# Optimization experiments

Measured on AMD Instinct MI355X. Metric: run time of the kernel, lower is better.

The kernel has to match this reference:

```python
import jax, jax.numpy as jnp
import numpy as np

B, CIN, COUT, K, H, W = 8, 256, 256, 4, 128, 128
BN_EPS = 1e-5


def setup_inputs() -> dict:
    key = jax.random.key(0)
    ks = jax.random.split(key, 12)
    n = lambda i, shape, scale: jax.random.normal(ks[i], shape, jnp.float32) * scale
    return {
        "x": jax.random.normal(ks[0], (B, CIN, H, W), jnp.float32),
        "conv_w": n(1, (COUT, CIN), 0.05),
        "conv_b": n(2, (COUT,), 0.02),
        "off_w": n(3, (K, 2, CIN), 0.02),   # k offset convs, each 1x1 -> 2 channels
        "off_b": n(4, (K, 2), 0.02),
        "wgt_w": n(5, (K, CIN), 0.05),      # weight conv 1x1 -> k channels (softmax over k)
        "wgt_b": n(6, (K,), 0.02),
        "gamma": 1.0 + n(7, (COUT,), 0.1),
        "beta": n(8, (COUT,), 0.1),
        "run_mean": n(9, (COUT,), 0.05),
        "run_var": 1.0 + 0.1 * jax.random.uniform(ks[10], (COUT,), jnp.float32),
        "out_w": n(11, (CIN, COUT), 0.05),
        "out_b": jnp.zeros((CIN,), jnp.float32),
    }


def bilinear_sample(img, gx, gy):
    """F.grid_sample(mode='bilinear', padding_mode='zeros', align_corners=True).
    img: [B,C,H,W]; gx,gy: [B,H,W] normalized coords in [-1,1]."""
    b, c, h, w = img.shape
    x = (gx + 1.0) * 0.5 * (w - 1)  # unnormalize (align_corners=True)
    y = (gy + 1.0) * 0.5 * (h - 1)
    x0 = jnp.floor(x)
    y0 = jnp.floor(y)
    wx1 = x - x0
    wy1 = y - y0
    imgf = img.reshape(b, c, h * w)

    def gather(xi, yi, wgt):
        valid = (xi >= 0) & (xi <= w - 1) & (yi >= 0) & (yi <= h - 1)
        xic = jnp.clip(xi, 0, w - 1).astype(jnp.int32)
        yic = jnp.clip(yi, 0, h - 1).astype(jnp.int32)
        idx = (yic * w + xic).reshape(b, 1, h * w)
        v = jnp.take_along_axis(imgf, idx, axis=2).reshape(b, c, h, w)
        return v * (wgt * valid)[:, None]  # zeros padding: OOB corners contribute 0

    return (gather(x0, y0, (1 - wx1) * (1 - wy1))
            + gather(x0 + 1, y0, wx1 * (1 - wy1))
            + gather(x0, y0 + 1, (1 - wx1) * wy1)
            + gather(x0 + 1, y0 + 1, wx1 * wy1))


def reference(x, conv_w, conv_b, off_w, off_b, wgt_w, wgt_b,
              gamma, beta, run_mean, run_var, out_w, out_b):
    # 1x1 projection conv
    proj = jnp.einsum('bchw,oc->bohw', x, conv_w) + conv_b[:, None, None]
    # k offset branches at once: [K,B,2,H,W]
    flows = jnp.einsum('bchw,koc->kbohw', x, off_w) + off_b[:, None, :, None, None]
    # per-branch softmax weights: [B,K,H,W]
    logits = jnp.einsum('bchw,kc->bkhw', x, wgt_w) + wgt_b[None, :, None, None]
    weights = jax.nn.softmax(logits, axis=1)
    # base grid + flow, normalized to [-1,1]
    grid_x = jnp.arange(W, dtype=jnp.float32)[None, None, None, :]  # broadcast over k,b,h
    grid_y = jnp.arange(H, dtype=jnp.float32)[None, None, :, None]
    vx = grid_x + flows[:, :, 0]  # [K,B,H,W]
    vy = grid_y + flows[:, :, 1]
    gxn = 2.0 * vx / max(W - 1, 1) - 1.0
    gyn = 2.0 * vy / max(H - 1, 1) - 1.0
    feats = jax.vmap(lambda gx, gy: bilinear_sample(proj, gx, gy))(gxn, gyn)  # [K,B,C,H,W]
    # repeat_interleave(weights, out_ch) * cat(feats) then split+sum == weighted sum over k
    fsum = jnp.einsum('kbchw,bkhw->bchw', feats, weights)
    feat = proj + fsum  # dropout in eval mode = identity
    # BatchNorm2d (eval: running stats)
    inv = gamma / jnp.sqrt(run_var + BN_EPS)
    feat = (feat - run_mean[:, None, None]) * inv[:, None, None] + beta[:, None, None]
    return jnp.einsum('bchw,oc->bohw', feat, out_w) + out_b[:, None, None]
```

## Files before the change

### kernel.cpp

```cpp
#include <hip/hip_runtime.h>
#include <cstddef>
#include <cstdint>

#define B_    8
#define CIN_  256
#define COUT_ 256
#define K_    4
#define H_    128
#define W_    128
#define HW_   (H_ * W_)
#define P_    (B_ * HW_)
#define BN_EPS 1e-5f

typedef __attribute__((ext_vector_type(8))) short bf16x8_t;
typedef __attribute__((ext_vector_type(4))) float f32x4_t;

__device__ __forceinline__ unsigned short f2bf(float f) {
    unsigned int u = __float_as_uint(f);
    u += 0x7fffu + ((u >> 16) & 1u);
    return (unsigned short)(u >> 16);
}
__device__ __forceinline__ float2 up2(unsigned int u) {
    return make_float2(__uint_as_float(u << 16), __uint_as_float(u & 0xffff0000u));
}
__device__ __forceinline__ void fma2(float2& d, float s, float2 v) {
    d.x = fmaf(s, v.x, d.x);
    d.y = fmaf(s, v.y, d.y);
}

#define GL2LDS(g, l)                                                                     \
    __builtin_amdgcn_global_load_lds((const __attribute__((address_space(1))) void*)(g), \
                                     (__attribute__((address_space(3))) void*)(l), 16, 0, 0)

__global__ __launch_bounds__(256) void k_prep(
    const float* __restrict__ conv_w, const float* __restrict__ out_w,
    const float* __restrict__ gamma, const float* __restrict__ beta,
    const float* __restrict__ rmean, const float* __restrict__ rvar,
    const float* __restrict__ out_b,
    unsigned short* __restrict__ wA, unsigned short* __restrict__ wB,
    float* __restrict__ bias2)
{
    const int t = threadIdx.x;
    if (blockIdx.x < 64) {
        const int i = (blockIdx.x * 256 + t) * 4;
        float4 a = *(const float4*)&conv_w[i];
        uint2 pa;
        pa.x = (unsigned)f2bf(a.x) | ((unsigned)f2bf(a.y) << 16);
        pa.y = (unsigned)f2bf(a.z) | ((unsigned)f2bf(a.w) << 16);
        *(uint2*)&wA[i] = pa;
    } else {
        __shared__ float sinv[256], sd[256];
        const float iv = gamma[t] * rsqrtf(rvar[t] + BN_EPS);
        sinv[t] = iv;
        sd[t]   = beta[t] - rmean[t] * iv;
        __syncthreads();
        float acc = out_b[t];
        for (int c = 0; c < 256; c += 4) {
            const float4 wv = *(const float4*)&out_w[t * 256 + c];
            acc += sd[c] * wv.x + sd[c + 1] * wv.y + sd[c + 2] * wv.z + sd[c + 3] * wv.w;
            uint2 p;
            p.x = (unsigned)f2bf(wv.x * sinv[c])     | ((unsigned)f2bf(wv.y * sinv[c + 1]) << 16);
            p.y = (unsigned)f2bf(wv.z * sinv[c + 2]) | ((unsigned)f2bf(wv.w * sinv[c + 3]) << 16);
            *(uint2*)&wB[t * 256 + c] = p;
        }
        bias2[t] = acc;
    }
}

__global__ __launch_bounds__(256) void k_flows(
    const float* __restrict__ x, const float* __restrict__ off_w,
    const float* __restrict__ off_b, const float* __restrict__ wgt_w,
    const float* __restrict__ wgt_b, unsigned short* __restrict__ xT,
    float4* __restrict__ tabW, int4* __restrict__ tabI)
{
    __shared__ float coef[12 * 256];
    __shared__ alignas(16) unsigned short tile[256 * 68];
    const int t = threadIdx.x;
    for (int idx = t; idx < 12 * 256; idx += 256)
        coef[idx] = (idx < 8 * 256) ? off_w[idx] : wgt_w[idx - 8 * 256];
    __syncthreads();

    const int p  = blockIdx.x * 256 + t;
    const int b  = p >> 14;
    const int hw = p & (HW_ - 1);
    const float* xp = x + (size_t)b * (256 * HW_) + hw;
    const int px0 = blockIdx.x * 256;

    float acc[12];
#pragma unroll
    for (int j = 0; j < 12; ++j) acc[j] = 0.f;

    for (int chunk = 0; chunk < 4; ++chunk) {
        const int cbase = chunk * 64;
#pragma unroll 4
        for (int cc = 0; cc < 64; ++cc) {
            const float xv = xp[(size_t)(cbase + cc) * HW_];
            tile[t * 68 + cc] = f2bf(xv);
#pragma unroll
            for (int j = 0; j < 12; ++j)
                acc[j] = fmaf(xv, coef[j * 256 + cbase + cc], acc[j]);
        }
        __syncthreads();
#pragma unroll
        for (int pass = 0; pass < 16; ++pass) {
            const int px = pass * 16 + (t >> 4);
            const int j4 = (t & 15) * 4;
            const uint2 v = *(const uint2*)&tile[px * 68 + j4];
            *(uint2*)&xT[(size_t)(px0 + px) * 256 + cbase + j4] = v;
        }
        __syncthreads();
    }

    const int w = hw & (W_ - 1);
    const int h = hw >> 7;
    float l[4];
#pragma unroll
    for (int k = 0; k < 4; ++k) l[k] = acc[8 + k] + wgt_b[k];
    const float m  = fmaxf(fmaxf(l[0], l[1]), fmaxf(l[2], l[3]));
    const float e0 = __expf(l[0] - m), e1 = __expf(l[1] - m);
    const float e2 = __expf(l[2] - m), e3 = __expf(l[3] - m);
    const float sinv = 1.f / (e0 + e1 + e2 + e3);
    float wk[4] = {e0 * sinv, e1 * sinv, e2 * sinv, e3 * sinv};

#pragma unroll
    for (int k = 0; k < 4; ++k) {
        const float sx = (float)w + acc[k * 2 + 0] + off_b[k * 2 + 0];
        const float sy = (float)h + acc[k * 2 + 1] + off_b[k * 2 + 1];
        const float x0f = floorf(sx), y0f = floorf(sy);
        const float fx = sx - x0f, fy = sy - y0f;
        const float vx0 = (x0f >= 0.f  && x0f <= (float)(W_ - 1)) ? 1.f : 0.f;
        const float vx1 = (x0f >= -1.f && x0f <= (float)(W_ - 2)) ? 1.f : 0.f;
        const float vy0 = (y0f >= 0.f  && y0f <= (float)(H_ - 1)) ? 1.f : 0.f;
        const float vy1 = (y0f >= -1.f && y0f <= (float)(H_ - 2)) ? 1.f : 0.f;
        const int x0 = (int)x0f, y0 = (int)y0f;
        const int cx0 = min(max(x0, 0), W_ - 1);
        const int cx1 = min(max(x0 + 1, 0), W_ - 1);
        const int cy0 = min(max(y0, 0), H_ - 1);
        const int cy1 = min(max(y0 + 1, 0), H_ - 1);
        float4 wv;
        wv.x = (1.f - fx) * (1.f - fy) * wk[k] * vx0 * vy0;
        wv.y = fx * (1.f - fy) * wk[k] * vx1 * vy0;
        wv.z = (1.f - fx) * fy * wk[k] * vx0 * vy1;
        wv.w = fx * fy * wk[k] * vx1 * vy1;
        int4 ov;
        ov.x = (cy0 * W_ + cx0) * 256;
        ov.y = (cy0 * W_ + cx1) * 256;
        ov.z = (cy1 * W_ + cx0) * 256;
        ov.w = (cy1 * W_ + cx1) * 256;
        tabW[(size_t)k * P_ + p] = wv;
        tabI[(size_t)k * P_ + p] = ov;
    }
}

#define GEMM_STAGE_AND_MFMA(A_, W_ptr_, smem_)                                              \
    char* As = smem_;                                                                       \
    char* Bs = smem_ + 16384;                                                               \
    const int w  = t >> 6;                                                                  \
    const int l  = t & 63;                                                                  \
    const int lr = l & 15;                                                                  \
    const int lq = l >> 4;                                                                  \
    f32x4_t acc[4][4];                                                                      \
    _Pragma("unroll") for (int i = 0; i < 4; ++i)                                           \
        _Pragma("unroll") for (int j = 0; j < 4; ++j)                                       \
            acc[i][j] = (f32x4_t){0.f, 0.f, 0.f, 0.f};                                      \
    const int wm = (w & 1) * 4;                                                             \
    const int wn = (w >> 1) * 4;                                                            \
    _Pragma("unroll") for (int ks = 0; ks < 4; ++ks) {                                      \
        const int k0 = ks * 64;                                                             \
        __syncthreads();                                                                    \
        _Pragma("unroll") for (int i = 0; i < 2; ++i) {                                     \
            const int mt = 2 * w + i;                                                       \
            _Pragma("unroll") for (int kc = 0; kc < 2; ++kc) {                              \
                const unsigned short* g =                                                   \
                    A_ + (size_t)(p0 + mt * 16 + lr) * 256 + k0 + kc * 32 + lq * 8;         \
                GL2LDS(g, As + (kc * 8 + mt) * 1024);                                       \
            }                                                                               \
        }                                                                                   \
        _Pragma("unroll") for (int i = 0; i < 2; ++i) {                                     \
            const int nt = 2 * w + i;                                                       \
            _Pragma("unroll") for (int kc = 0; kc < 2; ++kc) {                              \
                const unsigned short* g =                                                   \
                    W_ptr_ + (size_t)(n0 + nt * 16 + lr) * 256 + k0 + kc * 32 + lq * 8;     \
                GL2LDS(g, Bs + (kc * 8 + nt) * 1024);                                       \
            }                                                                               \
        }                                                                                   \
        __syncthreads();                                                                    \
        _Pragma("unroll") for (int kc = 0; kc < 2; ++kc) {                                  \
            bf16x8_t af[4], bfr[4];                                                         \
            _Pragma("unroll") for (int i = 0; i < 4; ++i)                                   \
                af[i] = *(const bf16x8_t*)(As + (kc * 8 + wm + i) * 1024 + l * 16);         \
            _Pragma("unroll") for (int j = 0; j < 4; ++j)                                   \
                bfr[j] = *(const bf16x8_t*)(Bs + (kc * 8 + wn + j) * 1024 + l * 16);        \
            _Pragma("unroll") for (int i = 0; i < 4; ++i)                                   \
                _Pragma("unroll") for (int j = 0; j < 4; ++j)                               \
                    acc[i][j] =                                                             \
                        __builtin_amdgcn_mfma_f32_16x16x32_bf16(af[i], bfr[j], acc[i][j],   \
                                                                0, 0, 0);                   \
        }                                                                                   \
    }

__global__ __launch_bounds__(256, 3) void k_proj(
    const unsigned short* __restrict__ A, const unsigned short* __restrict__ Wb,
    const float* __restrict__ bias, unsigned short* __restrict__ Cout)
{
    __shared__ alignas(16) char smem[33792];
    const int t  = threadIdx.x;
    const int bx = blockIdx.x;
    const int n0 = (bx & 1) * 128;
    const int p0 = (bx >> 1) * 128;

    GEMM_STAGE_AND_MFMA(A, Wb, smem)

    __syncthreads();
    unsigned short* ep = (unsigned short*)smem;
    const int mh = (w & 1) * 64, nh = (w >> 1) * 64;
#pragma unroll
    for (int j = 0; j < 4; ++j) {
        const int   col = nh + j * 16 + lr;
        const float bv  = bias[n0 + col];
#pragma unroll
        for (int i = 0; i < 4; ++i) {
#pragma unroll
            for (int r = 0; r < 4; ++r) {
                const int row = mh + i * 16 + lq * 4 + r;
                ep[row * 132 + col] = f2bf(acc[i][j][r] + bv);
            }
        }
    }
    __syncthreads();
#pragma unroll
    for (int pass = 0; pass < 16; ++pass) {
        const int row = pass * 8 + (t >> 5);
        const int c4  = (t & 31) * 4;
        const uint2 v = *(const uint2*)&ep[row * 132 + c4];
        *(uint2*)&Cout[(size_t)(p0 + row) * 256 + n0 + c4] = v;
    }
}

__global__ __launch_bounds__(256, 3) void k_out(
    const unsigned short* __restrict__ A, const unsigned short* __restrict__ Wb,
    const float* __restrict__ bias, float* __restrict__ Cout)
{
    __shared__ alignas(16) char smem[32768];
    const int t  = threadIdx.x;
    const int bx = blockIdx.x;
    const int n0 = (bx & 1) * 128;
    const int p0 = (bx >> 1) * 128;

    GEMM_STAGE_AND_MFMA(A, Wb, smem)

    const int mh = (w & 1) * 64, nh = (w >> 1) * 64;
    const int b   = p0 >> 14;
    const int hw0 = p0 & (HW_ - 1);
#pragma unroll
    for (int j = 0; j < 4; ++j) {
        const int   n  = n0 + nh + j * 16 + lr;
        const float bb = bias[n];
#pragma unroll
        for (int i = 0; i < 4; ++i) {
            f32x4_t v = acc[i][j];
            v[0] += bb; v[1] += bb; v[2] += bb; v[3] += bb;
            *(f32x4_t*)&Cout[(size_t)(b * 256 + n) * HW_ + hw0 + mh + i * 16 + lq * 4] = v;
        }
    }
}

__global__ __launch_bounds__(256) void k_sample(
    const unsigned short* __restrict__ proj, const float4* __restrict__ tabW,
    const int4* __restrict__ tabI, unsigned short* __restrict__ feat)
{
    const int t  = threadIdx.x;
    const int w  = t >> 6;
    const int l  = t & 63;
    const int ph = l >> 5;
    const int c0 = (l & 31) * 8;

    const int pbase = blockIdx.x * 16;
    const int b = pbase >> 14;
    const unsigned short* projb = proj + (size_t)b * HW_ * 256;

#pragma unroll
    for (int it = 0; it < 2; ++it) {
        const int p = pbase + it * 8 + w * 2 + ph;
        const uint4 rv = *(const uint4*)&proj[(size_t)p * 256 + c0];
        float2 a0 = up2(rv.x), a1 = up2(rv.y), a2 = up2(rv.z), a3 = up2(rv.w);
#pragma unroll
        for (int k = 0; k < 4; ++k) {
            const float4 wv = tabW[(size_t)k * P_ + p];
            const int4   ov = tabI[(size_t)k * P_ + p];
            const uint4 g0 = *(const uint4*)&projb[ov.x + c0];
            const uint4 g1 = *(const uint4*)&projb[ov.y + c0];
            const uint4 g2 = *(const uint4*)&projb[ov.z + c0];
            const uint4 g3 = *(const uint4*)&projb[ov.w + c0];
            fma2(a0, wv.x, up2(g0.x)); fma2(a1, wv.x, up2(g0.y));
            fma2(a2, wv.x, up2(g0.z)); fma2(a3, wv.x, up2(g0.w));
            fma2(a0, wv.y, up2(g1.x)); fma2(a1, wv.y, up2(g1.y));
            fma2(a2, wv.y, up2(g1.z)); fma2(a3, wv.y, up2(g1.w));
            fma2(a0, wv.z, up2(g2.x)); fma2(a1, wv.z, up2(g2.y));
            fma2(a2, wv.z, up2(g2.z)); fma2(a3, wv.z, up2(g2.w));
            fma2(a0, wv.w, up2(g3.x)); fma2(a1, wv.w, up2(g3.y));
            fma2(a2, wv.w, up2(g3.z)); fma2(a3, wv.w, up2(g3.w));
        }
        uint4 o;
        o.x = (unsigned)f2bf(a0.x) | ((unsigned)f2bf(a0.y) << 16);
        o.y = (unsigned)f2bf(a1.x) | ((unsigned)f2bf(a1.y) << 16);
        o.z = (unsigned)f2bf(a2.x) | ((unsigned)f2bf(a2.y) << 16);
        o.w = (unsigned)f2bf(a3.x) | ((unsigned)f2bf(a3.y) << 16);
        *(uint4*)&feat[(size_t)p * 256 + c0] = o;
    }
}

extern "C" void kernel_launch(void* const* d_in, const int* in_sizes, int n_in,
                              void* d_out, int out_size, void* d_ws, size_t ws_size,
                              hipStream_t stream)
{
    const float* x      = (const float*)d_in[0];
    const float* conv_w = (const float*)d_in[1];
    const float* conv_b = (const float*)d_in[2];
    const float* off_w  = (const float*)d_in[3];
    const float* off_b  = (const float*)d_in[4];
    const float* wgt_w  = (const float*)d_in[5];
    const float* wgt_b  = (const float*)d_in[6];
    const float* gamma  = (const float*)d_in[7];
    const float* beta   = (const float*)d_in[8];
    const float* rmean  = (const float*)d_in[9];
    const float* rvar   = (const float*)d_in[10];
    const float* out_w  = (const float*)d_in[11];
    const float* out_b  = (const float*)d_in[12];

    char* ws = (char*)d_ws;
    unsigned short* xT   = (unsigned short*)(ws);
    unsigned short* proj = (unsigned short*)(ws + (size_t)67108864);
    unsigned short* feat = (unsigned short*)(ws + (size_t)134217728);
    float4*         tabW = (float4*)(ws + (size_t)201326592);
    int4*           tabI = (int4*)(ws + (size_t)209715200);
    unsigned short* wA   = (unsigned short*)(ws + (size_t)218103808);
    unsigned short* wB   = (unsigned short*)(ws + (size_t)218234880);
    float*          bias2= (float*)(ws + (size_t)218365952);

    k_prep  <<<65,         256, 0, stream>>>(conv_w, out_w, gamma, beta, rmean, rvar,
                                             out_b, wA, wB, bias2);
    k_flows <<<P_ / 256,   256, 0, stream>>>(x, off_w, off_b, wgt_w, wgt_b, xT, tabW, tabI);
    k_proj  <<<(P_/128)*2, 256, 0, stream>>>(xT, wA, conv_b, proj);
    k_sample<<<P_ / 16,    256, 0, stream>>>(proj, tabW, tabI, feat);
    k_out   <<<(P_/128)*2, 256, 0, stream>>>(feat, wB, bias2, (float*)d_out);
}
```

Before: 427.9 us.

## Split channel reduction across four wave groups in k_flows and drop the LDS transpose

k_flows now handles 64 pixels per block. Each of the four wavefronts reduces a different 16-channel slice, and the partial sums for the 12 offset and weight dot products are combined through shared memory. Each thread converts its 16 channels to bf16 and writes them to xT as two 16-byte stores, which replaces the shared-memory tile transpose and its barriers. This raises parallelism and cuts LDS traffic in the stage that reads x. In exchange it adds a cross-wave reduction, lets only one wave finish the tail computation, and makes global stores less coalesced since each lane writes 32 bytes at a 512-byte stride.

```diff
diff --git a/kernel.cpp b/kernel.cpp
--- a/kernel.cpp
+++ b/kernel.cpp
@@ -73,82 +73,105 @@
     const float* __restrict__ wgt_b, unsigned short* __restrict__ xT,
     float4* __restrict__ tabW, int4* __restrict__ tabI)
 {
-    __shared__ float coef[12 * 256];
-    __shared__ alignas(16) unsigned short tile[256 * 68];
+    __shared__ float smem[3456];
     const int t = threadIdx.x;
     for (int idx = t; idx < 12 * 256; idx += 256)
-        coef[idx] = (idx < 8 * 256) ? off_w[idx] : wgt_w[idx - 8 * 256];
-    __syncthreads();
-
-    const int p  = blockIdx.x * 256 + t;
-    const int b  = p >> 14;
-    const int hw = p & (HW_ - 1);
+        smem[idx] = (idx < 8 * 256) ? off_w[idx] : wgt_w[idx - 8 * 256];
+    __syncthreads();
+
+    const int px  = t & 63;
+    const int grp = t >> 6;
+    const int p   = blockIdx.x * 64 + px;
+    const int b   = p >> 14;
+    const int hw  = p & (HW_ - 1);
     const float* xp = x + (size_t)b * (256 * HW_) + hw;
-    const int px0 = blockIdx.x * 256;
+    unsigned short* xtp = xT + (size_t)p * 256;
 
     float acc[12];
 #pragma unroll
     for (int j = 0; j < 12; ++j) acc[j] = 0.f;
 
+#pragma unroll
     for (int chunk = 0; chunk < 4; ++chunk) {
-        const int cbase = chunk * 64;
-#pragma unroll 4
-        for (int cc = 0; cc < 64; ++cc) {
-            const float xv = xp[(size_t)(cbase + cc) * HW_];
-            tile[t * 68 + cc] = f2bf(xv);
+        const int cbase = chunk * 64 + grp * 16;
+        float xv[16];
+#pragma unroll
+        for (int i = 0; i < 16; ++i)
+            xv[i] = xp[(size_t)(cbase + i) * HW_];
+
+        uint4 u0, u1;
+        u0.x = (unsigned)f2bf(xv[0])  | ((unsigned)f2bf(xv[1])  << 16);
+        u0.y = (unsigned)f2bf(xv[2])  | ((unsigned)f2bf(xv[3])  << 16);
+        u0.z = (unsigned)f2bf(xv[4])  | ((unsigned)f2bf(xv[5])  << 16);
+        u0.w = (unsigned)f2bf(xv[6])  | ((unsigned)f2bf(xv[7])  << 16);
+        u1.x = (unsigned)f2bf(xv[8])  | ((unsigned)f2bf(xv[9])  << 16);
+        u1.y = (unsigned)f2bf(xv[10]) | ((unsigned)f2bf(xv[11]) << 16);
+        u1.z = (unsigned)f2bf(xv[12]) | ((unsigned)f2bf(xv[13]) << 16);
+        u1.w = (unsigned)f2bf(xv[14]) | ((unsigned)f2bf(xv[15]) << 16);
+        *(uint4*)&xtp[cbase]     = u0;
+        *(uint4*)&xtp[cbase + 8] = u1;
+
+#pragma unroll
+        for (int i = 0; i < 16; ++i) {
 #pragma unroll
             for (int j = 0; j < 12; ++j)
-                acc[j] = fmaf(xv, coef[j * 256 + cbase + cc], acc[j]);
-        }
-        __syncthreads();
-#pragma unroll
-        for (int pass = 0; pass < 16; ++pass) {
-            const int px = pass * 16 + (t >> 4);
-            const int j4 = (t & 15) * 4;
-            const uint2 v = *(const uint2*)&tile[px * 68 + j4];
-            *(uint2*)&xT[(size_t)(px0 + px) * 256 + cbase + j4] = v;
-        }
-        __syncthreads();
-    }
-
-    const int w = hw & (W_ - 1);
-    const int h = hw >> 7;
-    float l[4];
-#pragma unroll
-    for (int k = 0; k < 4; ++k) l[k] = acc[8 + k] + wgt_b[k];
-    const float m  = fmaxf(fmaxf(l[0], l[1]), fmaxf(l[2], l[3]));
-    const float e0 = __expf(l[0] - m), e1 = __expf(l[1] - m);
-    const float e2 = __expf(l[2] - m), e3 = __expf(l[3] - m);
-    const float sinv = 1.f / (e0 + e1 + e2 + e3);
-    float wk[4] = {e0 * sinv, e1 * sinv, e2 * sinv, e3 * sinv};
-
-#pragma unroll
-    for (int k = 0; k < 4; ++k) {
-        const float sx = (float)w + acc[k * 2 + 0] + off_b[k * 2 + 0];
-        const float sy = (float)h + acc[k * 2 + 1] + off_b[k * 2 + 1];
-        const float x0f = floorf(sx), y0f = floorf(sy);
-        const float fx = sx - x0f, fy = sy - y0f;
-        const float vx0 = (x0f >= 0.f  && x0f <= (float)(W_ - 1)) ? 1.f : 0.f;
-        const float vx1 = (x0f >= -1.f && x0f <= (float)(W_ - 2)) ? 1.f : 0.f;
-        const float vy0 = (y0f >= 0.f  && y0f <= (float)(H_ - 1)) ? 1.f : 0.f;
-        const float vy1 = (y0f >= -1.f && y0f <= (float)(H_ - 2)) ? 1.f : 0.f;
-        const int x0 = (int)x0f, y0 = (int)y0f;
-        const int cx0 = min(max(x0, 0), W_ - 1);
-        const int cx1 = min(max(x0 + 1, 0), W_ - 1);
-        const int cy0 = min(max(y0, 0), H_ - 1);
-        const int cy1 = min(max(y0 + 1, 0), H_ - 1);
-        float4 wv;
-        wv.x = (1.f - fx) * (1.f - fy) * wk[k] * vx0 * vy0;
-        wv.y = fx * (1.f - fy) * wk[k] * vx1 * vy0;
-        wv.z = (1.f - fx) * fy * wk[k] * vx0 * vy1;
-        wv.w = fx * fy * wk[k] * vx1 * vy1;
-        int4 ov;
-        ov.x = (cy0 * W_ + cx0) * 256;
-        ov.y = (cy0 * W_ + cx1) * 256;
-        ov.z = (cy1 * W_ + cx0) * 256;
-        ov.w = (cy1 * W_ + cx1) * 256;
-        tabW[(size_t)k * P_ + p] = wv;
-        tabI[(size_t)k * P_ + p] = ov;
+                acc[j] = fmaf(xv[i], smem[j * 256 + cbase + i], acc[j]);
+        }
+    }
+
+    __syncthreads();
+    float* red = smem;
+#pragma unroll
+    for (int j = 0; j < 12; ++j)
+        red[(grp * 64 + px) * 13 + j] = acc[j];
+    __syncthreads();
+
+    if (t < 64) {
+        float a[12];
+#pragma unroll
+        for (int j = 0; j < 12; ++j)
+            a[j] = (red[(0 * 64 + t) * 13 + j] + red[(1 * 64 + t) * 13 + j])
+                 + (red[(2 * 64 + t) * 13 + j] + red[(3 * 64 + t) * 13 + j]);
+
+        const int w = hw & (W_ - 1);
+        const int h = hw >> 7;
+        float l[4];
+#pragma unroll
+        for (int k = 0; k < 4; ++k) l[k] = a[8 + k] + wgt_b[k];
+        const float m  = fmaxf(fmaxf(l[0], l[1]), fmaxf(l[2], l[3]));
+        const float e0 = __expf(l[0] - m), e1 = __expf(l[1] - m);
+        const float e2 = __expf(l[2] - m), e3 = __expf(l[3] - m);
+        const float sinv = 1.f / (e0 + e1 + e2 + e3);
+        float wk[4] = {e0 * sinv, e1 * sinv, e2 * sinv, e3 * sinv};
+
+#pragma unroll
+        for (int k = 0; k < 4; ++k) {
+            const float sx = (float)w + a[k * 2 + 0] + off_b[k * 2 + 0];
+            const float sy = (float)h + a[k * 2 + 1] + off_b[k * 2 + 1];
+            const float x0f = floorf(sx), y0f = floorf(sy);
+            const float fx = sx - x0f, fy = sy - y0f;
+            const float vx0 = (x0f >= 0.f  && x0f <= (float)(W_ - 1)) ? 1.f : 0.f;
+            const float vx1 = (x0f >= -1.f && x0f <= (float)(W_ - 2)) ? 1.f : 0.f;
+            const float vy0 = (y0f >= 0.f  && y0f <= (float)(H_ - 1)) ? 1.f : 0.f;
+            const float vy1 = (y0f >= -1.f && y0f <= (float)(H_ - 2)) ? 1.f : 0.f;
+            const int x0 = (int)x0f, y0 = (int)y0f;
+            const int cx0 = min(max(x0, 0), W_ - 1);
+            const int cx1 = min(max(x0 + 1, 0), W_ - 1);
+            const int cy0 = min(max(y0, 0), H_ - 1);
+            const int cy1 = min(max(y0 + 1, 0), H_ - 1);
+            float4 wv;
+            wv.x = (1.f - fx) * (1.f - fy) * wk[k] * vx0 * vy0;
+            wv.y = fx * (1.f - fy) * wk[k] * vx1 * vy0;
+            wv.z = (1.f - fx) * fy * wk[k] * vx0 * vy1;
+            wv.w = fx * fy * wk[k] * vx1 * vy1;
+            int4 ov;
+            ov.x = (cy0 * W_ + cx0) * 256;
+            ov.y = (cy0 * W_ + cx1) * 256;
+            ov.z = (cy1 * W_ + cx0) * 256;
+            ov.w = (cy1 * W_ + cx1) * 256;
+            tabW[(size_t)k * P_ + p] = wv;
+            tabI[(size_t)k * P_ + p] = ov;
+        }
     }
 }
 
@@ -340,7 +363,7 @@
 
     k_prep  <<<65,         256, 0, stream>>>(conv_w, out_w, gamma, beta, rmean, rvar,
                                              out_b, wA, wB, bias2);
-    k_flows <<<P_ / 256,   256, 0, stream>>>(x, off_w, off_b, wgt_w, wgt_b, xT, tabW, tabI);
+    k_flows <<<P_ / 64,    256, 0, stream>>>(x, off_w, off_b, wgt_w, wgt_b, xT, tabW, tabI);
     k_proj  <<<(P_/128)*2, 256, 0, stream>>>(xT, wA, conv_b, proj);
     k_sample<<<P_ / 16,    256, 0, stream>>>(proj, tabW, tabI, feat);
     k_out   <<<(P_/128)*2, 256, 0, stream>>>(feat, wB, bias2, (float*)d_out);
```

Measured after the change: 430.7 us. About the same (+0.7%).

## Vectorize k_flows loads, split channels across warp groups, drop smem transpose

Applied to the files above, without the earlier changes.

k_flows now has each thread load float4s covering 4 adjacent pixels. The four 64-thread groups each take a 16-channel slice of every 64-channel chunk. Each thread packs its pixels' channels to bf16 and writes the transposed xT directly as 16-byte stores, so the shared-memory tile transpose and its per-chunk barriers are gone. Partial offset and weight sums are reduced across groups through shared memory before the softmax and bilinear-table step. The xT stores are now strided by row per lane and each thread needs more registers, which could hurt write coalescing or occupancy.

```diff
diff --git a/kernel.cpp b/kernel.cpp
--- a/kernel.cpp
+++ b/kernel.cpp
@@ -73,82 +73,122 @@
     const float* __restrict__ wgt_b, unsigned short* __restrict__ xT,
     float4* __restrict__ tabW, int4* __restrict__ tabI)
 {
-    __shared__ float coef[12 * 256];
-    __shared__ alignas(16) unsigned short tile[256 * 68];
+    __shared__ float smem[4 * 64 * 49];
     const int t = threadIdx.x;
     for (int idx = t; idx < 12 * 256; idx += 256)
-        coef[idx] = (idx < 8 * 256) ? off_w[idx] : wgt_w[idx - 8 * 256];
-    __syncthreads();
-
-    const int p  = blockIdx.x * 256 + t;
-    const int b  = p >> 14;
-    const int hw = p & (HW_ - 1);
-    const float* xp = x + (size_t)b * (256 * HW_) + hw;
+        smem[idx] = (idx < 8 * 256) ? off_w[idx] : wgt_w[idx - 8 * 256];
+    __syncthreads();
+
+    const int q  = t & 63;
+    const int g  = t >> 6;
     const int px0 = blockIdx.x * 256;
-
-    float acc[12];
-#pragma unroll
-    for (int j = 0; j < 12; ++j) acc[j] = 0.f;
-
+    const int p4 = px0 + q * 4;
+    const int b  = p4 >> 14;
+    const float* xq = x + (size_t)b * (256 * HW_) + (p4 & (HW_ - 1));
+
+    float acc[12][4];
+#pragma unroll
+    for (int j = 0; j < 12; ++j)
+#pragma unroll
+        for (int o = 0; o < 4; ++o) acc[j][o] = 0.f;
+
+#pragma unroll
     for (int chunk = 0; chunk < 4; ++chunk) {
-        const int cbase = chunk * 64;
-#pragma unroll 4
-        for (int cc = 0; cc < 64; ++cc) {
-            const float xv = xp[(size_t)(cbase + cc) * HW_];
-            tile[t * 68 + cc] = f2bf(xv);
-#pragma unroll
-            for (int j = 0; j < 12; ++j)
-                acc[j] = fmaf(xv, coef[j * 256 + cbase + cc], acc[j]);
-        }
-        __syncthreads();
-#pragma unroll
-        for (int pass = 0; pass < 16; ++pass) {
-            const int px = pass * 16 + (t >> 4);
-            const int j4 = (t & 15) * 4;
-            const uint2 v = *(const uint2*)&tile[px * 68 + j4];
-            *(uint2*)&xT[(size_t)(px0 + px) * 256 + cbase + j4] = v;
-        }
-        __syncthreads();
-    }
-
-    const int w = hw & (W_ - 1);
-    const int h = hw >> 7;
-    float l[4];
-#pragma unroll
-    for (int k = 0; k < 4; ++k) l[k] = acc[8 + k] + wgt_b[k];
-    const float m  = fmaxf(fmaxf(l[0], l[1]), fmaxf(l[2], l[3]));
-    const float e0 = __expf(l[0] - m), e1 = __expf(l[1] - m);
-    const float e2 = __expf(l[2] - m), e3 = __expf(l[3] - m);
-    const float sinv = 1.f / (e0 + e1 + e2 + e3);
-    float wk[4] = {e0 * sinv, e1 * sinv, e2 * sinv, e3 * sinv};
-
-#pragma unroll
-    for (int k = 0; k < 4; ++k) {
-        const float sx = (float)w + acc[k * 2 + 0] + off_b[k * 2 + 0];
-        const float sy = (float)h + acc[k * 2 + 1] + off_b[k * 2 + 1];
-        const float x0f = floorf(sx), y0f = floorf(sy);
-        const float fx = sx - x0f, fy = sy - y0f;
-        const float vx0 = (x0f >= 0.f  && x0f <= (float)(W_ - 1)) ? 1.f : 0.f;
-        const float vx1 = (x0f >= -1.f && x0f <= (float)(W_ - 2)) ? 1.f : 0.f;
-        const float vy0 = (y0f >= 0.f  && y0f <= (float)(H_ - 1)) ? 1.f : 0.f;
-        const float vy1 = (y0f >= -1.f && y0f <= (float)(H_ - 2)) ? 1.f : 0.f;
-        const int x0 = (int)x0f, y0 = (int)y0f;
-        const int cx0 = min(max(x0, 0), W_ - 1);
-        const int cx1 = min(max(x0 + 1, 0), W_ - 1);
-        const int cy0 = min(max(y0, 0), H_ - 1);
-        const int cy1 = min(max(y0 + 1, 0), H_ - 1);
-        float4 wv;
-        wv.x = (1.f - fx) * (1.f - fy) * wk[k] * vx0 * vy0;
-        wv.y = fx * (1.f - fy) * wk[k] * vx1 * vy0;
-        wv.z = (1.f - fx) * fy * wk[k] * vx0 * vy1;
-        wv.w = fx * fy * wk[k] * vx1 * vy1;
-        int4 ov;
-        ov.x = (cy0 * W_ + cx0) * 256;
-        ov.y = (cy0 * W_ + cx1) * 256;
-        ov.z = (cy1 * W_ + cx0) * 256;
-        ov.w = (cy1 * W_ + cx1) * 256;
-        tabW[(size_t)k * P_ + p] = wv;
-        tabI[(size_t)k * P_ + p] = ov;
+        const int cbase = chunk * 64 + g * 16;
+#pragma unroll
+        for (int bb = 0; bb < 2; ++bb) {
+            float4 f4[8];
+#pragma unroll
+            for (int i = 0; i < 8; ++i)
+                f4[i] = *(const float4*)&xq[(size_t)(cbase + bb * 8 + i) * HW_];
+#pragma unroll
+            for (int i = 0; i < 8; ++i) {
+                const int ch = cbase + bb * 8 + i;
+#pragma unroll
+                for (int j = 0; j < 12; ++j) {
+                    const float cw = smem[j * 256 + ch];
+                    acc[j][0] = fmaf(f4[i].x, cw, acc[j][0]);
+                    acc[j][1] = fmaf(f4[i].y, cw, acc[j][1]);
+                    acc[j][2] = fmaf(f4[i].z, cw, acc[j][2]);
+                    acc[j][3] = fmaf(f4[i].w, cw, acc[j][3]);
+                }
+            }
+#pragma unroll
+            for (int o = 0; o < 4; ++o) {
+                const float vo[8] = {f4[0].x, f4[1].x, f4[2].x, f4[3].x,
+                                     f4[4].x, f4[5].x, f4[6].x, f4[7].x};
+                float v[8];
+#pragma unroll
+                for (int i = 0; i < 8; ++i)
+                    v[i] = (o == 0) ? f4[i].x : (o == 1) ? f4[i].y : (o == 2) ? f4[i].z : f4[i].w;
+                (void)vo;
+                uint4 u;
+                u.x = (unsigned)f2bf(v[0]) | ((unsigned)f2bf(v[1]) << 16);
+                u.y = (unsigned)f2bf(v[2]) | ((unsigned)f2bf(v[3]) << 16);
+                u.z = (unsigned)f2bf(v[4]) | ((unsigned)f2bf(v[5]) << 16);
+                u.w = (unsigned)f2bf(v[6]) | ((unsigned)f2bf(v[7]) << 16);
+                *(uint4*)&xT[(size_t)(p4 + o) * 256 + cbase + bb * 8] = u;
+            }
+        }
+    }
+
+    __syncthreads();
+#pragma unroll
+    for (int j = 0; j < 12; ++j)
+#pragma unroll
+        for (int o = 0; o < 4; ++o)
+            smem[(g * 64 + q) * 49 + j * 4 + o] = acc[j][o];
+    __syncthreads();
+
+    {
+        const int q2 = t >> 2, o2 = t & 3;
+        const int p  = px0 + t;
+        float a[12];
+#pragma unroll
+        for (int j = 0; j < 12; ++j)
+            a[j] = (smem[(0 * 64 + q2) * 49 + j * 4 + o2] + smem[(1 * 64 + q2) * 49 + j * 4 + o2])
+                 + (smem[(2 * 64 + q2) * 49 + j * 4 + o2] + smem[(3 * 64 + q2) * 49 + j * 4 + o2]);
+
+        const int hw = p & (HW_ - 1);
+        const int w = hw & (W_ - 1);
+        const int h = hw >> 7;
+        float l[4];
+#pragma unroll
+        for (int k = 0; k < 4; ++k) l[k] = a[8 + k] + wgt_b[k];
+        const float m  = fmaxf(fmaxf(l[0], l[1]), fmaxf(l[2], l[3]));
+        const float e0 = __expf(l[0] - m), e1 = __expf(l[1] - m);
+        const float e2 = __expf(l[2] - m), e3 = __expf(l[3] - m);
+        const float sinv = 1.f / (e0 + e1 + e2 + e3);
+        float wk[4] = {e0 * sinv, e1 * sinv, e2 * sinv, e3 * sinv};
+
+#pragma unroll
+        for (int k = 0; k < 4; ++k) {
+            const float sx = (float)w + a[k * 2 + 0] + off_b[k * 2 + 0];
+            const float sy = (float)h + a[k * 2 + 1] + off_b[k * 2 + 1];
+            const float x0f = floorf(sx), y0f = floorf(sy);
+            const float fx = sx - x0f, fy = sy - y0f;
+            const float vx0 = (x0f >= 0.f  && x0f <= (float)(W_ - 1)) ? 1.f : 0.f;
+            const float vx1 = (x0f >= -1.f && x0f <= (float)(W_ - 2)) ? 1.f : 0.f;
+            const float vy0 = (y0f >= 0.f  && y0f <= (float)(H_ - 1)) ? 1.f : 0.f;
+            const float vy1 = (y0f >= -1.f && y0f <= (float)(H_ - 2)) ? 1.f : 0.f;
+            const int x0 = (int)x0f, y0 = (int)y0f;
+            const int cx0 = min(max(x0, 0), W_ - 1);
+            const int cx1 = min(max(x0 + 1, 0), W_ - 1);
+            const int cy0 = min(max(y0, 0), H_ - 1);
+            const int cy1 = min(max(y0 + 1, 0), H_ - 1);
+            float4 wv;
+            wv.x = (1.f - fx) * (1.f - fy) * wk[k] * vx0 * vy0;
+            wv.y = fx * (1.f - fy) * wk[k] * vx1 * vy0;
+            wv.z = (1.f - fx) * fy * wk[k] * vx0 * vy1;
+            wv.w = fx * fy * wk[k] * vx1 * vy1;
+            int4 ov;
+            ov.x = (cy0 * W_ + cx0) * 256;
+            ov.y = (cy0 * W_ + cx1) * 256;
+            ov.z = (cy1 * W_ + cx0) * 256;
+            ov.w = (cy1 * W_ + cx1) * 256;
+            tabW[(size_t)k * P_ + p] = wv;
+            tabI[(size_t)k * P_ + p] = ov;
+        }
     }
 }
 
```

After: 451.1 us. 5.4% more time.

## Fuse flow/weight conv into projection GEMM, reading x directly without transposed copy

Applied to the files above, without the earlier changes.

Replaces the separate k_flows and k_proj kernels with a single k_fproj kernel. It loads fp32 x, converts it to bf16 into a swizzled LDS tile, and runs both the 256-channel projection GEMM and the 12-channel offset/weight conv (padded to 16, now computed in bf16 MFMA) from that one tile. The fused kernel then computes the softmax and bilinear tables. This drops the round trip of the xT intermediate through HBM and one kernel launch. The cost is that offset/logit precision falls from fp32 FMA to bf16 inputs, which can shift sample coordinates, and the larger 512-thread block uses more LDS.

```diff
diff --git a/kernel.cpp b/kernel.cpp
--- a/kernel.cpp
+++ b/kernel.cpp
@@ -36,9 +36,10 @@
     const float* __restrict__ conv_w, const float* __restrict__ out_w,
     const float* __restrict__ gamma, const float* __restrict__ beta,
     const float* __restrict__ rmean, const float* __restrict__ rvar,
-    const float* __restrict__ out_b,
+    const float* __restrict__ out_b, const float* __restrict__ off_w,
+    const float* __restrict__ wgt_w,
     unsigned short* __restrict__ wA, unsigned short* __restrict__ wB,
-    float* __restrict__ bias2)
+    float* __restrict__ bias2, unsigned short* __restrict__ wB2)
 {
     const int t = threadIdx.x;
     if (blockIdx.x < 64) {
@@ -48,7 +49,7 @@
         pa.x = (unsigned)f2bf(a.x) | ((unsigned)f2bf(a.y) << 16);
         pa.y = (unsigned)f2bf(a.z) | ((unsigned)f2bf(a.w) << 16);
         *(uint2*)&wA[i] = pa;
-    } else {
+    } else if (blockIdx.x == 64) {
         __shared__ float sinv[256], sd[256];
         const float iv = gamma[t] * rsqrtf(rvar[t] + BN_EPS);
         sinv[t] = iv;
@@ -64,91 +65,193 @@
             *(uint2*)&wB[t * 256 + c] = p;
         }
         bias2[t] = acc;
-    }
-}
-
-__global__ __launch_bounds__(256) void k_flows(
-    const float* __restrict__ x, const float* __restrict__ off_w,
-    const float* __restrict__ off_b, const float* __restrict__ wgt_w,
-    const float* __restrict__ wgt_b, unsigned short* __restrict__ xT,
-    float4* __restrict__ tabW, int4* __restrict__ tabI)
+    } else {
+        for (int j = 0; j < 16; ++j) {
+            float v = 0.f;
+            if (j < 8)       v = off_w[j * 256 + t];
+            else if (j < 12) v = wgt_w[(j - 8) * 256 + t];
+            wB2[j * 256 + t] = f2bf(v);
+        }
+    }
+}
+
+__global__ __launch_bounds__(512, 2) void k_fproj(
+    const float* __restrict__ x, const unsigned short* __restrict__ wA,
+    const unsigned short* __restrict__ wB2, const float* __restrict__ conv_b,
+    const float* __restrict__ off_b, const float* __restrict__ wgt_b,
+    unsigned short* __restrict__ proj, float4* __restrict__ tabW,
+    int4* __restrict__ tabI)
 {
-    __shared__ float coef[12 * 256];
-    __shared__ alignas(16) unsigned short tile[256 * 68];
-    const int t = threadIdx.x;
-    for (int idx = t; idx < 12 * 256; idx += 256)
-        coef[idx] = (idx < 8 * 256) ? off_w[idx] : wgt_w[idx - 8 * 256];
+    __shared__ alignas(16) char smem[57856];
+    char*           AsB  = smem;
+    char*           Bs   = smem + 16384;
+    float*          fbuf = (float*)(smem + 49152);
+    unsigned short* ep   = (unsigned short*)smem;
+
+    const int t   = threadIdx.x;
+    const int w   = t >> 6;
+    const int l   = t & 63;
+    const int lr  = l & 15;
+    const int lq  = l >> 4;
+    const int wm2 = w & 1;
+    const int wn4 = w >> 1;
+    const int chg = t & 15;
+    const int pxg = t >> 4;
+    const int p0  = blockIdx.x * 128;
+    const float* xb = x + (size_t)(p0 >> 14) * (256 * HW_) + (p0 & (HW_ - 1)) + pxg * 4;
+
+    f32x4_t acc[4][4];
+#pragma unroll
+    for (int i = 0; i < 4; ++i)
+#pragma unroll
+        for (int j = 0; j < 4; ++j) acc[i][j] = (f32x4_t){0.f, 0.f, 0.f, 0.f};
+    f32x4_t acc2 = (f32x4_t){0.f, 0.f, 0.f, 0.f};
+
+    float4 f[4], fn[4];
+#pragma unroll
+    for (int i = 0; i < 4; ++i)
+        f[i] = *(const float4*)&xb[(size_t)(chg * 4 + i) * HW_];
+
+    for (int ks = 0; ks < 4; ++ks) {
+#pragma unroll
+        for (int o = 0; o < 4; ++o) {
+            const int px = pxg * 4 + o;
+            const float v0 = (o == 0) ? f[0].x : (o == 1) ? f[0].y : (o == 2) ? f[0].z : f[0].w;
+            const float v1 = (o == 0) ? f[1].x : (o == 1) ? f[1].y : (o == 2) ? f[1].z : f[1].w;
+            const float v2 = (o == 0) ? f[2].x : (o == 1) ? f[2].y : (o == 2) ? f[2].z : f[2].w;
+            const float v3 = (o == 0) ? f[3].x : (o == 1) ? f[3].y : (o == 2) ? f[3].z : f[3].w;
+            uint2 u;
+            u.x = (unsigned)f2bf(v0) | ((unsigned)f2bf(v1) << 16);
+            u.y = (unsigned)f2bf(v2) | ((unsigned)f2bf(v3) << 16);
+            *(uint2*)(AsB + ((px * 128 + chg * 8) ^ ((px & 7) << 4))) = u;
+        }
+#pragma unroll
+        for (int s = 0; s < 4; ++s) {
+            const int idx = w * 4 + s;
+            const unsigned short* g = wA + (size_t)((idx & 15) * 16 + lr) * 256
+                                      + ks * 64 + (idx >> 4) * 32 + lq * 8;
+            GL2LDS(g, Bs + idx * 1024);
+        }
+        if (ks < 3) {
+#pragma unroll
+            for (int i = 0; i < 4; ++i)
+                fn[i] = *(const float4*)&xb[(size_t)((ks + 1) * 64 + chg * 4 + i) * HW_];
+        }
+        __syncthreads();
+        {
+            const int px = w * 16 + lr;
+#pragma unroll
+            for (int kc = 0; kc < 2; ++kc) {
+                const bf16x8_t a2 = *(const bf16x8_t*)(AsB +
+                    ((px * 128 + kc * 64 + lq * 16) ^ ((px & 7) << 4)));
+                const bf16x8_t b2 = *(const bf16x8_t*)&wB2[lr * 256 + ks * 64 + kc * 32 + lq * 8];
+                acc2 = __builtin_amdgcn_mfma_f32_16x16x32_bf16(a2, b2, acc2, 0, 0, 0);
+            }
+        }
+#pragma unroll
+        for (int kc = 0; kc < 2; ++kc) {
+            bf16x8_t af[4], bfr[4];
+#pragma unroll
+            for (int i = 0; i < 4; ++i) {
+                const int px = (wm2 * 4 + i) * 16 + lr;
+                af[i] = *(const bf16x8_t*)(AsB +
+                    ((px * 128 + kc * 64 + lq * 16) ^ ((px & 7) << 4)));
+            }
+#pragma unroll
+            for (int j = 0; j < 4; ++j)
+                bfr[j] = *(const bf16x8_t*)(Bs + (kc * 16 + wn4 * 4 + j) * 1024 + l * 16);
+#pragma unroll
+            for (int i = 0; i < 4; ++i)
+#pragma unroll
+                for (int j = 0; j < 4; ++j)
+                    acc[i][j] = __builtin_amdgcn_mfma_f32_16x16x32_bf16(af[i], bfr[j],
+                                                                        acc[i][j], 0, 0, 0);
+        }
+        __syncthreads();
+        if (ks < 3) {
+#pragma unroll
+            for (int i = 0; i < 4; ++i) f[i] = fn[i];
+        }
+    }
+
+#pragma unroll
+    for (int r = 0; r < 4; ++r)
+        fbuf[(w * 16 + lq * 4 + r) * 17 + lr] = acc2[r];
     __syncthreads();
 
-    const int p  = blockIdx.x * 256 + t;
-    const int b  = p >> 14;
-    const int hw = p & (HW_ - 1);
-    const float* xp = x + (size_t)b * (256 * HW_) + hw;
-    const int px0 = blockIdx.x * 256;
-
-    float acc[12];
-#pragma unroll
-    for (int j = 0; j < 12; ++j) acc[j] = 0.f;
-
-    for (int chunk = 0; chunk < 4; ++chunk) {
-        const int cbase = chunk * 64;
-#pragma unroll 4
-        for (int cc = 0; cc < 64; ++cc) {
-            const float xv = xp[(size_t)(cbase + cc) * HW_];
-            tile[t * 68 + cc] = f2bf(xv);
-#pragma unroll
-            for (int j = 0; j < 12; ++j)
-                acc[j] = fmaf(xv, coef[j * 256 + cbase + cc], acc[j]);
+    if (t < 128) {
+        const int p = p0 + t;
+        float a[12];
+#pragma unroll
+        for (int j = 0; j < 12; ++j) a[j] = fbuf[t * 17 + j];
+
+        const int hw = p & (HW_ - 1);
+        const int wx = hw & (W_ - 1);
+        const int hy = hw >> 7;
+        float lg[4];
+#pragma unroll
+        for (int k = 0; k < 4; ++k) lg[k] = a[8 + k] + wgt_b[k];
+        const float m  = fmaxf(fmaxf(lg[0], lg[1]), fmaxf(lg[2], lg[3]));
+        const float e0 = __expf(lg[0] - m), e1 = __expf(lg[1] - m);
+        const float e2 = __expf(lg[2] - m), e3 = __expf(lg[3] - m);
+        const float sinv = 1.f / (e0 + e1 + e2 + e3);
+        const float wk[4] = {e0 * sinv, e1 * sinv, e2 * sinv, e3 * sinv};
+
+#pragma unroll
+        for (int k = 0; k < 4; ++k) {
+            const float sx = (float)wx + a[k * 2 + 0] + off_b[k * 2 + 0];
+            const float sy = (float)hy + a[k * 2 + 1] + off_b[k * 2 + 1];
+            const float x0f = floorf(sx), y0f = floorf(sy);
+            const float fx = sx - x0f, fy = sy - y0f;
+            const float vx0 = (x0f >= 0.f  && x0f <= (float)(W_ - 1)) ? 1.f : 0.f;
+            const float vx1 = (x0f >= -1.f && x0f <= (float)(W_ - 2)) ? 1.f : 0.f;
+            const float vy0 = (y0f >= 0.f  && y0f <= (float)(H_ - 1)) ? 1.f : 0.f;
+            const float vy1 = (y0f >= -1.f && y0f <= (float)(H_ - 2)) ? 1.f : 0.f;
+            const int x0 = (int)x0f, y0 = (int)y0f;
+            const int cx0 = min(max(x0, 0), W_ - 1);
+            const int cx1 = min(max(x0 + 1, 0), W_ - 1);
+            const int cy0 = min(max(y0, 0), H_ - 1);
+            const int cy1 = min(max(y0 + 1, 0), H_ - 1);
+            float4 wv;
+            wv.x = (1.f - fx) * (1.f - fy) * wk[k] * vx0 * vy0;
+            wv.y = fx * (1.f - fy) * wk[k] * vx1 * vy0;
+            wv.z = (1.f - fx) * fy * wk[k] * vx0 * vy1;
+            wv.w = fx * fy * wk[k] * vx1 * vy1;
+            int4 ov;
+            ov.x = (cy0 * W_ + cx0) * 256;
+            ov.y = (cy0 * W_ + cx1) * 256;
+            ov.z = (cy1 * W_ + cx0) * 256;
+            ov.w = (cy1 * W_ + cx1) * 256;
+            tabW[(size_t)k * P_ + p] = wv;
+            tabI[(size_t)k * P_ + p] = ov;
+        }
+    }
+
+    for (int h = 0; h < 2; ++h) {
+        if ((wn4 >> 1) == h) {
+#pragma unroll
+            for (int j = 0; j < 4; ++j) {
+                const int ncol = wn4 * 64 + j * 16 + lr;
+                const float bv = conv_b[ncol];
+                const int cl = (wn4 & 1) * 64 + j * 16 + lr;
+#pragma unroll
+                for (int i = 0; i < 4; ++i)
+#pragma unroll
+                    for (int r = 0; r < 4; ++r) {
+                        const int row = (wm2 * 4 + i) * 16 + lq * 4 + r;
+                        ep[row * 132 + cl] = f2bf(acc[i][j][r] + bv);
+                    }
+            }
         }
         __syncthreads();
 #pragma unroll
-        for (int pass = 0; pass < 16; ++pass) {
-            const int px = pass * 16 + (t >> 4);
-            const int j4 = (t & 15) * 4;
-            const uint2 v = *(const uint2*)&tile[px * 68 + j4];
-            *(uint2*)&xT[(size_t)(px0 + px) * 256 + cbase + j4] = v;
+        for (int pass = 0; pass < 8; ++pass) {
+            const int row = pass * 16 + (t >> 5);
+            const int c4  = (t & 31) * 4;
+            const uint2 v = *(const uint2*)&ep[row * 132 + c4];
+            *(uint2*)&proj[(size_t)(p0 + row) * 256 + h * 128 + c4] = v;
         }
         __syncthreads();
-    }
-
-    const int w = hw & (W_ - 1);
-    const int h = hw >> 7;
-    float l[4];
-#pragma unroll
-    for (int k = 0; k < 4; ++k) l[k] = acc[8 + k] + wgt_b[k];
-    const float m  = fmaxf(fmaxf(l[0], l[1]), fmaxf(l[2], l[3]));
-    const float e0 = __expf(l[0] - m), e1 = __expf(l[1] - m);
-    const float e2 = __expf(l[2] - m), e3 = __expf(l[3] - m);
-    const float sinv = 1.f / (e0 + e1 + e2 + e3);
-    float wk[4] = {e0 * sinv, e1 * sinv, e2 * sinv, e3 * sinv};
-
-#pragma unroll
-    for (int k = 0; k < 4; ++k) {
-        const float sx = (float)w + acc[k * 2 + 0] + off_b[k * 2 + 0];
-        const float sy = (float)h + acc[k * 2 + 1] + off_b[k * 2 + 1];
-        const float x0f = floorf(sx), y0f = floorf(sy);
-        const float fx = sx - x0f, fy = sy - y0f;
-        const float vx0 = (x0f >= 0.f  && x0f <= (float)(W_ - 1)) ? 1.f : 0.f;
-        const float vx1 = (x0f >= -1.f && x0f <= (float)(W_ - 2)) ? 1.f : 0.f;
-        const float vy0 = (y0f >= 0.f  && y0f <= (float)(H_ - 1)) ? 1.f : 0.f;
-        const float vy1 = (y0f >= -1.f && y0f <= (float)(H_ - 2)) ? 1.f : 0.f;
-        const int x0 = (int)x0f, y0 = (int)y0f;
-        const int cx0 = min(max(x0, 0), W_ - 1);
-        const int cx1 = min(max(x0 + 1, 0), W_ - 1);
-        const int cy0 = min(max(y0, 0), H_ - 1);
-        const int cy1 = min(max(y0 + 1, 0), H_ - 1);
-        float4 wv;
-        wv.x = (1.f - fx) * (1.f - fy) * wk[k] * vx0 * vy0;
-        wv.y = fx * (1.f - fy) * wk[k] * vx1 * vy0;
-        wv.z = (1.f - fx) * fy * wk[k] * vx0 * vy1;
-        wv.w = fx * fy * wk[k] * vx1 * vy1;
-        int4 ov;
-        ov.x = (cy0 * W_ + cx0) * 256;
-        ov.y = (cy0 * W_ + cx1) * 256;
-        ov.z = (cy1 * W_ + cx0) * 256;
-        ov.w = (cy1 * W_ + cx1) * 256;
-        tabW[(size_t)k * P_ + p] = wv;
-        tabI[(size_t)k * P_ + p] = ov;
     }
 }
 
@@ -199,44 +302,6 @@
         }                                                                                   \
     }
 
-__global__ __launch_bounds__(256, 3) void k_proj(
-    const unsigned short* __restrict__ A, const unsigned short* __restrict__ Wb,
-    const float* __restrict__ bias, unsigned short* __restrict__ Cout)
-{
-    __shared__ alignas(16) char smem[33792];
-    const int t  = threadIdx.x;
-    const int bx = blockIdx.x;
-    const int n0 = (bx & 1) * 128;
-    const int p0 = (bx >> 1) * 128;
-
-    GEMM_STAGE_AND_MFMA(A, Wb, smem)
-
-    __syncthreads();
-    unsigned short* ep = (unsigned short*)smem;
-    const int mh = (w & 1) * 64, nh = (w >> 1) * 64;
-#pragma unroll
-    for (int j = 0; j < 4; ++j) {
-        const int   col = nh + j * 16 + lr;
-        const float bv  = bias[n0 + col];
-#pragma unroll
-        for (int i = 0; i < 4; ++i) {
-#pragma unroll
-            for (int r = 0; r < 4; ++r) {
-                const int row = mh + i * 16 + lq * 4 + r;
-                ep[row * 132 + col] = f2bf(acc[i][j][r] + bv);
-            }
-        }
-    }
-    __syncthreads();
-#pragma unroll
-    for (int pass = 0; pass < 16; ++pass) {
-        const int row = pass * 8 + (t >> 5);
-        const int c4  = (t & 31) * 4;
-        const uint2 v = *(const uint2*)&ep[row * 132 + c4];
-        *(uint2*)&Cout[(size_t)(p0 + row) * 256 + n0 + c4] = v;
-    }
-}
-
 __global__ __launch_bounds__(256, 3) void k_out(
     const unsigned short* __restrict__ A, const unsigned short* __restrict__ Wb,
     const float* __restrict__ bias, float* __restrict__ Cout)
@@ -329,7 +394,7 @@
     const float* out_b  = (const float*)d_in[12];
 
     char* ws = (char*)d_ws;
-    unsigned short* xT   = (unsigned short*)(ws);
+    unsigned short* wB2  = (unsigned short*)(ws);
     unsigned short* proj = (unsigned short*)(ws + (size_t)67108864);
     unsigned short* feat = (unsigned short*)(ws + (size_t)134217728);
     float4*         tabW = (float4*)(ws + (size_t)201326592);
@@ -338,10 +403,10 @@
     unsigned short* wB   = (unsigned short*)(ws + (size_t)218234880);
     float*          bias2= (float*)(ws + (size_t)218365952);
 
-    k_prep  <<<65,         256, 0, stream>>>(conv_w, out_w, gamma, beta, rmean, rvar,
-                                             out_b, wA, wB, bias2);
-    k_flows <<<P_ / 256,   256, 0, stream>>>(x, off_w, off_b, wgt_w, wgt_b, xT, tabW, tabI);
-    k_proj  <<<(P_/128)*2, 256, 0, stream>>>(xT, wA, conv_b, proj);
+    k_prep  <<<66,         256, 0, stream>>>(conv_w, out_w, gamma, beta, rmean, rvar,
+                                             out_b, off_w, wgt_w, wA, wB, bias2, wB2);
+    k_fproj <<<P_ / 128,   512, 0, stream>>>(x, wA, wB2, conv_b, off_b, wgt_b,
+                                             proj, tabW, tabI);
     k_sample<<<P_ / 16,    256, 0, stream>>>(proj, tabW, tabI, feat);
     k_out   <<<(P_/128)*2, 256, 0, stream>>>(feat, wB, bias2, (float*)d_out);
 }
```

Measured after the change: 392.5 us. -8.3%, faster.
